# Kernel optimization log

Measured on AMD Instinct MI355X. Metric: run time of the kernel, lower is better.

## Reference

```python
import jax, jax.numpy as jnp
import numpy as np

B = 16384  # batch size
NP = 49    # 7x7 patches


def _attn(Q, K, V):
    # Faithful to the torch loop: token[i] = Q[i].T @ K[i] / sqrt(S) @ V[i].T, then permute.
    # Note dk = Q.size(1) == 49 (seq len), NOT the head dim — preserved here.
    scale = 1.0 / jnp.asarray(Q.shape[1], Q.dtype) ** 0.5  # 1/7
    S = jnp.einsum('bsd,bse->bde', Q, K) * scale           # (B, d, d)
    # (S @ V^T)^T  ->  out[b,s,d] = sum_e S[b,d,e] * V[b,s,e]
    return jnp.einsum('bde,bse->bsd', S, V)                # (B, 49, d)


def setup_inputs() -> dict:
    key = jax.random.key(0)
    ks = jax.random.split(key, 12)
    s = 0.1  # init scale for weights
    return {
        'x':       jax.random.normal(ks[0], (B, 3, 28, 28), dtype=jnp.float32),
        'pos_emb': jax.random.uniform(ks[1], (7, 7, 16), dtype=jnp.float32),  # torch.rand
        'WQ1': jax.random.normal(ks[2], (NP, 16, 32), dtype=jnp.float32) * s,
        'WK1': jax.random.normal(ks[3], (NP, 16, 32), dtype=jnp.float32) * s,
        'WV1': jax.random.normal(ks[4], (NP, 16, 32), dtype=jnp.float32) * s,
        'WQ2': jax.random.normal(ks[5], (NP, 8, 16), dtype=jnp.float32) * s,
        'WK2': jax.random.normal(ks[6], (NP, 8, 16), dtype=jnp.float32) * s,
        'WV2': jax.random.normal(ks[7], (NP, 8, 16), dtype=jnp.float32) * s,
        'fc1_w': jax.random.normal(ks[8], (16, NP * 8), dtype=jnp.float32) * s,
        'fc1_b': jnp.zeros((16,), dtype=jnp.float32),
        'fc2_w': jax.random.normal(ks[9], (10, 16), dtype=jnp.float32) * s,
        'fc2_b': jnp.zeros((10,), dtype=jnp.float32),
    }


def reference(x, pos_emb, WQ1, WK1, WV1, WQ2, WK2, WV2, fc1_w, fc1_b, fc2_w, fc2_b):
    b = x.shape[0]
    # grayscale (x has 3 channels)
    g = 0.299 * x[:, 0] + 0.587 * x[:, 1] + 0.114 * x[:, 2]   # (B, 28, 28)
    # 7x7 grid of 4x4 patches, flattened row-major within each patch
    patches = g.reshape(b, 7, 4, 7, 4).transpose(0, 1, 3, 2, 4).reshape(b, NP, 16)
    pe = jnp.broadcast_to(pos_emb.reshape(1, NP, 16), (b, NP, 16))
    tok1 = jnp.concatenate([patches, pe], axis=-1)            # (B, 49, 32)

    # 49 independent per-patch projections, batched: y[:,s,:] = tok[:,s,:] @ W[s].T
    Q1 = jnp.einsum('bsi,soi->bso', tok1, WQ1)
    K1 = jnp.einsum('bsi,soi->bso', tok1, WK1)
    V1 = jnp.einsum('bsi,soi->bso', tok1, WV1)
    tok2 = jax.nn.softmax(_attn(Q1, K1, V1), axis=-1)         # (B, 49, 16)

    Q2 = jnp.einsum('bsi,soi->bso', tok2, WQ2)
    K2 = jnp.einsum('bsi,soi->bso', tok2, WK2)
    V2 = jnp.einsum('bsi,soi->bso', tok2, WV2)
    tok3 = jax.nn.softmax(_attn(Q2, K2, V2), axis=-1)         # (B, 49, 8)

    flat = tok3.reshape(b, NP * 8)
    h = jax.nn.relu(flat @ fc1_w.T + fc1_b)
    return jax.nn.softmax(h @ fc2_w.T + fc2_b, axis=-1)       # (B, 10)
```

## Files before the change

kernel.cpp:

```cpp
#include <hip/hip_runtime.h>
#include <cstdint>

typedef unsigned int u32;
typedef unsigned short u16;
typedef _Float16 h2 __attribute__((ext_vector_type(2)));

#define WS_W1A   0
#define WS_W1B   37632
#define WS_CQ    75264
#define WS_W2A   84672
#define WS_W2B   103488
#define WS_F1H   122304
#define WS_F1B   134848
#define WS_F2W   134912
#define WS_F2B   135552

__device__ __forceinline__ u32 packh2(float a, float b) {
  h2 h; h.x = (_Float16)a; h.y = (_Float16)b;
  return __builtin_bit_cast(u32, h);
}
__device__ __forceinline__ float dot2u(u32 a, u32 b, float c) {
#if __has_builtin(__builtin_amdgcn_fdot2)
  return __builtin_amdgcn_fdot2(__builtin_bit_cast(h2, a), __builtin_bit_cast(h2, b), c, false);
#else
  h2 ha = __builtin_bit_cast(h2, a), hb = __builtin_bit_cast(h2, b);
  return c + (float)ha.x * (float)hb.x + (float)ha.y * (float)hb.y;
#endif
}
__device__ __forceinline__ float dot16(const u32* t, uint4 a, uint4 b, float c) {
  c = dot2u(t[0], a.x, c); c = dot2u(t[1], a.y, c);
  c = dot2u(t[2], a.z, c); c = dot2u(t[3], a.w, c);
  c = dot2u(t[4], b.x, c); c = dot2u(t[5], b.y, c);
  c = dot2u(t[6], b.z, c); c = dot2u(t[7], b.w, c);
  return c;
}

__device__ __forceinline__ void wfence() {
  __builtin_amdgcn_sched_barrier(0);
  asm volatile("s_waitcnt lgkmcnt(0)" ::: "memory");
  __builtin_amdgcn_sched_barrier(0);
}

extern "C" __global__ void vit_prep(
    const float* __restrict__ pe,
    const float* __restrict__ wq1, const float* __restrict__ wk1, const float* __restrict__ wv1,
    const float* __restrict__ wq2, const float* __restrict__ wk2, const float* __restrict__ wv2,
    const float* __restrict__ fw1, const float* __restrict__ fb1,
    const float* __restrict__ fw2, const float* __restrict__ fb2,
    char* __restrict__ ws)
{
  const int t = blockIdx.x * 256 + threadIdx.x;
  _Float16* w1aH = (_Float16*)(ws + WS_W1A);
  _Float16* w1bH = (_Float16*)(ws + WS_W1B);
  float*    cq   = (float*)(ws + WS_CQ);
  _Float16* w2aH = (_Float16*)(ws + WS_W2A);
  _Float16* w2bH = (_Float16*)(ws + WS_W2B);
  u32* f1h = (u32*)(ws + WS_F1H);
  float* o1b = (float*)(ws + WS_F1B);
  float* o2w = (float*)(ws + WS_F2W);
  float* o2b = (float*)(ws + WS_F2B);

  if (t < 2352) {
    int p = t / 784, rem = t % 784;
    int o = rem / 49, s = rem % 49;
    const float* W = (p == 0 ? wq1 : (p == 1 ? wk1 : wv1)) + s*512 + o*32;
    float sc = (p == 0) ? (1.0f/7.0f) : 1.0f;
    #pragma unroll
    for (int i = 0; i < 8; ++i) w1aH[t*8 + i] = (_Float16)(W[i] * sc);
    #pragma unroll
    for (int i = 0; i < 8; ++i) w1bH[t*8 + i] = (_Float16)(W[8 + i] * sc);
    float acc = 0.f;
    #pragma unroll
    for (int i = 0; i < 16; ++i) acc += pe[s*16 + i] * W[16 + i];
    cq[t] = acc * sc;
  } else if (t < 3528) {
    int u = t - 2352;
    int p = u / 392, rem = u % 392;
    int o = rem / 49, s = rem % 49;
    const float* W = (p == 0 ? wq2 : (p == 1 ? wk2 : wv2)) + s*128 + o*16;
    float sc = (p == 0) ? (1.0f/7.0f) : 1.0f;
    #pragma unroll
    for (int i = 0; i < 8; ++i) w2aH[u*8 + i] = (_Float16)(W[i] * sc);
    #pragma unroll
    for (int i = 0; i < 8; ++i) w2bH[u*8 + i] = (_Float16)(W[8 + i] * sc);
  } else if (t < 6664) {
    int u = t - 3528;
    int h = u / 196, jc = u % 196;
    f1h[u] = packh2(fw1[h*392 + 2*jc], fw1[h*392 + 2*jc + 1]);
  } else if (t < 6680) {
    int u = t - 6664; o1b[u] = fb1[u];
  } else if (t < 6840) {
    int u = t - 6680; o2w[u] = fw2[u];
  } else if (t < 6850) {
    int u = t - 6840; o2b[u] = fb2[u];
  }
}

extern "C" __global__ void __launch_bounds__(256, 2)
vit_main(const float* __restrict__ x, const char* __restrict__ ws, float* __restrict__ out)
{
  __shared__ uint4 smem4[32768 / 16];
  char* smem = (char*)smem4;
  const u32 tid  = threadIdx.x;
  const u32 lane = tid & 63u;
  const u32 wv   = tid >> 6;

  const uint4* g1a = (const uint4*)(ws + WS_W1A);
  const uint4* g1b = (const uint4*)(ws + WS_W1B);
  const float* gcq = (const float*)(ws + WS_CQ);
  const uint4* g2a = (const uint4*)(ws + WS_W2A);
  const uint4* g2b = (const uint4*)(ws + WS_W2B);
  const uint4* f1hg = (const uint4*)(ws + WS_F1H);
  const float* f1bg = (const float*)(ws + WS_F1B);
  const float* f2wg = (const float*)(ws + WS_F2W);
  const float* f2bg = (const float*)(ws + WS_F2B);

  char* pw = smem + wv * 8192;
  const u32 s = lane;
  const u32 pr = s / 7u, pc = s - pr * 7u;

  const u32 bbase = blockIdx.x * 8u + wv * 2u;

  u32 p2h[2][8];
  u32 v1h[2][8];
  u32 th4[2][8];
  u32 v2h[2][4];

  if (s < 49u) {
    #pragma unroll
    for (int u = 0; u < 2; ++u) {
      const float* xb = x + (size_t)(bbase + u) * 2352u;
      #pragma unroll
      for (int r = 0; r < 4; ++r) {
        const float* rp = xb + (4u*pr + r) * 28u + 4u*pc;
        float4 rr = *(const float4*)rp;
        float4 gg = *(const float4*)(rp + 784);
        float4 bb = *(const float4*)(rp + 1568);
        float g0 = 0.299f*rr.x + 0.587f*gg.x + 0.114f*bb.x;
        float g1 = 0.299f*rr.y + 0.587f*gg.y + 0.114f*bb.y;
        float g2 = 0.299f*rr.z + 0.587f*gg.z + 0.114f*bb.z;
        float g3 = 0.299f*rr.w + 0.587f*gg.w + 0.114f*bb.w;
        p2h[u][r*2]   = packh2(g0, g1);
        p2h[u][r*2+1] = packh2(g2, g3);
      }
    }
  }

  if (s < 49u) {
    const int si = (int)s;
    uint4 qa0, qb0, qa1, qb1; float qc0, qc1;
    uint4 ka0, kb0, ka1, kb1; float kc0, kc1;
    uint4 va0, vb0, va1, vb1; float vc0, vc1;
#define LDQ1(OP) { const int r0 = (OP)*98 + si;        qa0=g1a[r0]; qb0=g1b[r0]; qa1=g1a[r0+49]; qb1=g1b[r0+49]; qc0=gcq[r0]; qc1=gcq[r0+49]; }
#define LDK1(OP) { const int r0 = (OP)*98 + si + 784;  ka0=g1a[r0]; kb0=g1b[r0]; ka1=g1a[r0+49]; kb1=g1b[r0+49]; kc0=gcq[r0]; kc1=gcq[r0+49]; }
#define LDV1(OP) { const int r0 = (OP)*98 + si + 1568; va0=g1a[r0]; vb0=g1b[r0]; va1=g1a[r0+49]; vb1=g1b[r0+49]; vc0=gcq[r0]; vc1=gcq[r0+49]; }
    LDQ1(0); LDK1(0); LDV1(0);
    #pragma unroll
    for (int op = 0; op < 8; ++op) {
      const int o = 2*op;
      {
        #pragma unroll
        for (int u = 0; u < 2; ++u) {
          _Float16* qrow = (_Float16*)(pw + u*4096);
          qrow[o*56 + s]     = (_Float16)dot16(p2h[u], qa0, qb0, qc0);
          qrow[(o+1)*56 + s] = (_Float16)dot16(p2h[u], qa1, qb1, qc1);
        }
      }
      if (op < 7) LDQ1(op+1);
      {
        #pragma unroll
        for (int u = 0; u < 2; ++u) {
          _Float16* krow = (_Float16*)(pw + u*4096 + 1792);
          krow[o*56 + s]     = (_Float16)dot16(p2h[u], ka0, kb0, kc0);
          krow[(o+1)*56 + s] = (_Float16)dot16(p2h[u], ka1, kb1, kc1);
        }
      }
      if (op < 7) LDK1(op+1);
      {
        #pragma unroll
        for (int u = 0; u < 2; ++u)
          v1h[u][op] = packh2(dot16(p2h[u], va0, vb0, vc0), dot16(p2h[u], va1, vb1, vc1));
      }
      if (op < 7) LDV1(op+1);
    }
#undef LDQ1
#undef LDK1
#undef LDV1
  }
  wfence();

  {
    const u32 d2 = lane >> 3, e2 = lane & 7u;
    #pragma unroll
    for (int u = 0; u < 2; ++u) {
      char* su = pw + u*4096;
      const u32* qw = (const u32*)su;
      const u32* kw = (const u32*)(su + 1792);
      const u32* qA = qw + (2u*d2) * 28u;
      const u32* qB = qA + 28u;
      const u32* kA = kw + (2u*e2) * 28u;
      const u32* kB = kA + 28u;
      float a00 = 0.f, a01 = 0.f, a10 = 0.f, a11 = 0.f;
      #pragma unroll
      for (int t7 = 0; t7 < 6; ++t7) {
        uint4 qa = *(const uint4*)(qA + 4*t7);
        uint4 qb = *(const uint4*)(qB + 4*t7);
        uint4 ka = *(const uint4*)(kA + 4*t7);
        uint4 kb = *(const uint4*)(kB + 4*t7);
        a00 = dot2u(qa.x, ka.x, a00); a00 = dot2u(qa.y, ka.y, a00);
        a00 = dot2u(qa.z, ka.z, a00); a00 = dot2u(qa.w, ka.w, a00);
        a01 = dot2u(qa.x, kb.x, a01); a01 = dot2u(qa.y, kb.y, a01);
        a01 = dot2u(qa.z, kb.z, a01); a01 = dot2u(qa.w, kb.w, a01);
        a10 = dot2u(qb.x, ka.x, a10); a10 = dot2u(qb.y, ka.y, a10);
        a10 = dot2u(qb.z, ka.z, a10); a10 = dot2u(qb.w, ka.w, a10);
        a11 = dot2u(qb.x, kb.x, a11); a11 = dot2u(qb.y, kb.y, a11);
        a11 = dot2u(qb.z, kb.z, a11); a11 = dot2u(qb.w, kb.w, a11);
      }
      {
        float q0t = (float)((const _Float16*)qA)[48];
        float q1t = (float)((const _Float16*)qB)[48];
        float k0t = (float)((const _Float16*)kA)[48];
        float k1t = (float)((const _Float16*)kB)[48];
        a00 = fmaf(q0t, k0t, a00); a01 = fmaf(q0t, k1t, a01);
        a10 = fmaf(q1t, k0t, a10); a11 = fmaf(q1t, k1t, a11);
      }
      u32* s1 = (u32*)(su + 3584);
      s1[(2u*d2)*8u + e2]   = packh2(a00, a01);
      s1[(2u*d2+1)*8u + e2] = packh2(a10, a11);
    }
  }
  wfence();

  if (s < 49u) {
    #pragma unroll
    for (int u = 0; u < 2; ++u) {
      char* su = pw + u*4096;
      const u32* s1 = (const u32*)(su + 3584);
      float od[16];
      #pragma unroll
      for (int d = 0; d < 16; ++d) {
        uint4 sa = *(const uint4*)&s1[d*8];
        uint4 sb = *(const uint4*)&s1[d*8 + 4];
        float acc = dot2u(sa.x, v1h[u][0], 0.f);
        acc = dot2u(sa.y, v1h[u][1], acc);
        acc = dot2u(sa.z, v1h[u][2], acc);
        acc = dot2u(sa.w, v1h[u][3], acc);
        acc = dot2u(sb.x, v1h[u][4], acc);
        acc = dot2u(sb.y, v1h[u][5], acc);
        acc = dot2u(sb.z, v1h[u][6], acc);
        acc = dot2u(sb.w, v1h[u][7], acc);
        od[d] = acc;
      }
      float m = od[0];
      #pragma unroll
      for (int d = 1; d < 16; ++d) m = fmaxf(m, od[d]);
      float sum = 0.f;
      #pragma unroll
      for (int d = 0; d < 16; ++d) { od[d] = __expf(od[d] - m); sum += od[d]; }
      float rs = 1.0f / sum;
      #pragma unroll
      for (int j = 0; j < 8; ++j) th4[u][j] = packh2(od[2*j]*rs, od[2*j+1]*rs);
    }
  }

  if (s < 49u) {
    const int si = (int)s;
    uint4 qa0, qb0, qa1, qb1;
    uint4 ka0, kb0, ka1, kb1;
    uint4 va0, vb0, va1, vb1;
#define LDQ2(OP) { const int r0 = (OP)*98 + si;       qa0=g2a[r0]; qb0=g2b[r0]; qa1=g2a[r0+49]; qb1=g2b[r0+49]; }
#define LDK2(OP) { const int r0 = (OP)*98 + si + 392; ka0=g2a[r0]; kb0=g2b[r0]; ka1=g2a[r0+49]; kb1=g2b[r0+49]; }
#define LDV2(OP) { const int r0 = (OP)*98 + si + 784; va0=g2a[r0]; vb0=g2b[r0]; va1=g2a[r0+49]; vb1=g2b[r0+49]; }
    LDQ2(0); LDK2(0); LDV2(0);
    #pragma unroll
    for (int op = 0; op < 4; ++op) {
      const int o = 2*op;
      {
        #pragma unroll
        for (int u = 0; u < 2; ++u) {
          _Float16* qrow = (_Float16*)(pw + u*4096);
          qrow[o*56 + s]     = (_Float16)dot16(th4[u], qa0, qb0, 0.f);
          qrow[(o+1)*56 + s] = (_Float16)dot16(th4[u], qa1, qb1, 0.f);
        }
      }
      if (op < 3) LDQ2(op+1);
      {
        #pragma unroll
        for (int u = 0; u < 2; ++u) {
          _Float16* krow = (_Float16*)(pw + u*4096 + 896);
          krow[o*56 + s]     = (_Float16)dot16(th4[u], ka0, kb0, 0.f);
          krow[(o+1)*56 + s] = (_Float16)dot16(th4[u], ka1, kb1, 0.f);
        }
      }
      if (op < 3) LDK2(op+1);
      {
        #pragma unroll
        for (int u = 0; u < 2; ++u)
          v2h[u][op] = packh2(dot16(th4[u], va0, vb0, 0.f), dot16(th4[u], va1, vb1, 0.f));
      }
      if (op < 3) LDV2(op+1);
    }
#undef LDQ2
#undef LDK2
#undef LDV2
  }
  wfence();

  {
    const u32 uu = lane >> 5, d = (lane >> 2) & 7u, e2 = lane & 3u;
    char* su = pw + uu*4096;
    const u32* qw = (const u32*)su;
    const u32* kw = (const u32*)(su + 896);
    const u32* qA = qw + d * 28u;
    const u32* kA = kw + (2u*e2) * 28u;
    const u32* kB = kA + 28u;
    float a0 = 0.f, a1 = 0.f;
    #pragma unroll
    for (int t7 = 0; t7 < 6; ++t7) {
      uint4 qa = *(const uint4*)(qA + 4*t7);
      uint4 ka = *(const uint4*)(kA + 4*t7);
      uint4 kb = *(const uint4*)(kB + 4*t7);
      a0 = dot2u(qa.x, ka.x, a0); a0 = dot2u(qa.y, ka.y, a0);
      a0 = dot2u(qa.z, ka.z, a0); a0 = dot2u(qa.w, ka.w, a0);
      a1 = dot2u(qa.x, kb.x, a1); a1 = dot2u(qa.y, kb.y, a1);
      a1 = dot2u(qa.z, kb.z, a1); a1 = dot2u(qa.w, kb.w, a1);
    }
    {
      float qt = (float)((const _Float16*)qA)[48];
      float k0t = (float)((const _Float16*)kA)[48];
      float k1t = (float)((const _Float16*)kB)[48];
      a0 = fmaf(qt, k0t, a0); a1 = fmaf(qt, k1t, a1);
    }
    u32* s2 = (u32*)(su + 3584);
    s2[d*4u + e2] = packh2(a0, a1);
  }
  wfence();

  if (s < 49u) {
    #pragma unroll
    for (int u = 0; u < 2; ++u) {
      char* su = pw + u*4096;
      const u32* s2 = (const u32*)(su + 3584);
      float od[8];
      #pragma unroll
      for (int d = 0; d < 8; ++d) {
        uint4 sr = *(const uint4*)&s2[d*4];
        float acc = dot2u(sr.x, v2h[u][0], 0.f);
        acc = dot2u(sr.y, v2h[u][1], acc);
        acc = dot2u(sr.z, v2h[u][2], acc);
        acc = dot2u(sr.w, v2h[u][3], acc);
        od[d] = acc;
      }
      float m = od[0];
      #pragma unroll
      for (int d = 1; d < 8; ++d) m = fmaxf(m, od[d]);
      float sum = 0.f;
      #pragma unroll
      for (int d = 0; d < 8; ++d) { od[d] = __expf(od[d] - m); sum += od[d]; }
      float rs = 1.0f / sum;
      uint4 tw;
      tw.x = packh2(od[0]*rs, od[1]*rs);
      tw.y = packh2(od[2]*rs, od[3]*rs);
      tw.z = packh2(od[4]*rs, od[5]*rs);
      tw.w = packh2(od[6]*rs, od[7]*rs);
      *(uint4*)((u32*)su + s*4u) = tw;
    }
  }
  wfence();

  {
    const u32 uu = lane >> 5, h = (lane >> 1) & 15u, half = lane & 1u;
    char* su = pw + uu*4096;
    const u32* t3 = (const u32*)su;
    float acc = half ? 0.f : f1bg[h];
    #pragma unroll
    for (int jj = 0; jj < 25; ++jj) {
      int j = (int)(half * 25u) + jj;
      if (j < 49) {
        uint4 tj = *(const uint4*)&t3[j*4];
        uint4 wj = f1hg[h*49u + (u32)j];
        acc = dot2u(tj.x, wj.x, acc);
        acc = dot2u(tj.y, wj.y, acc);
        acc = dot2u(tj.z, wj.z, acc);
        acc = dot2u(tj.w, wj.w, acc);
      }
    }
    float* prt = (float*)(su + 3584 + 192);
    prt[h*2u + half] = acc;
  }
  wfence();

  {
    const u32 uu = lane >> 5, c = lane & 31u;
    char* su = pw + uu*4096;
    if (c < 10u) {
      const float4* pv4 = (const float4*)(su + 3584 + 192);
      float hb[16];
      #pragma unroll
      for (int g = 0; g < 8; ++g) {
        float4 pv = pv4[g];
        hb[2*g]   = fmaxf(pv.x + pv.y, 0.f);
        hb[2*g+1] = fmaxf(pv.z + pv.w, 0.f);
      }
      const float* wr = f2wg + c*16u;
      float acc = f2bg[c];
      #pragma unroll
      for (int h = 0; h < 16; ++h) acc = fmaf(hb[h], wr[h], acc);
      float* lg = (float*)(su + 3584 + 384);
      lg[c] = acc;
    }
  }
  wfence();

  {
    const u32 uu = lane >> 5, c = lane & 31u;
    char* su = pw + uu*4096;
    if (c < 10u) {
      const float* lg = (const float*)(su + 3584 + 384);
      float mx = lg[0];
      #pragma unroll
      for (int i = 1; i < 10; ++i) mx = fmaxf(mx, lg[i]);
      float sum = 0.f;
      #pragma unroll
      for (int i = 0; i < 10; ++i) sum += __expf(lg[i] - mx);
      out[(size_t)(bbase + uu) * 10u + c] = __expf(lg[c] - mx) / sum;
    }
  }
}

extern "C" void kernel_launch(void* const* d_in, const int* in_sizes, int n_in,
                              void* d_out, int out_size, void* d_ws, size_t ws_size,
                              hipStream_t stream)
{
  const float* x   = (const float*)d_in[0];
  const float* pe  = (const float*)d_in[1];
  const float* wq1 = (const float*)d_in[2];
  const float* wk1 = (const float*)d_in[3];
  const float* wv1 = (const float*)d_in[4];
  const float* wq2 = (const float*)d_in[5];
  const float* wk2 = (const float*)d_in[6];
  const float* wv2 = (const float*)d_in[7];
  const float* f1w = (const float*)d_in[8];
  const float* f1b = (const float*)d_in[9];
  const float* f2w = (const float*)d_in[10];
  const float* f2b = (const float*)d_in[11];
  char* ws = (char*)d_ws;
  float* out = (float*)d_out;

  hipLaunchKernelGGL(vit_prep, dim3(27), dim3(256), 0, stream,
                     pe, wq1, wk1, wv1, wq2, wk2, wv2, f1w, f1b, f2w, f2b, ws);
  hipLaunchKernelGGL(vit_main, dim3(2048), dim3(256), 0, stream, x, ws, out);
}
```

Measured before the change: 282.6 us.

## Process one sample per wavefront to cut registers and raise occupancy

```diff
diff --git a/kernel.cpp b/kernel.cpp
--- a/kernel.cpp
+++ b/kernel.cpp
@@ -96,10 +96,10 @@
   }
 }
 
-extern "C" __global__ void __launch_bounds__(256, 2)
+extern "C" __global__ void __launch_bounds__(256, 8)
 vit_main(const float* __restrict__ x, const char* __restrict__ ws, float* __restrict__ out)
 {
-  __shared__ uint4 smem4[32768 / 16];
+  __shared__ uint4 smem4[16384 / 16];
   char* smem = (char*)smem4;
   const u32 tid  = threadIdx.x;
   const u32 lane = tid & 63u;
@@ -115,34 +115,31 @@
   const float* f2wg = (const float*)(ws + WS_F2W);
   const float* f2bg = (const float*)(ws + WS_F2B);
 
-  char* pw = smem + wv * 8192;
+  char* su = smem + wv * 4096;
   const u32 s = lane;
   const u32 pr = s / 7u, pc = s - pr * 7u;
 
-  const u32 bbase = blockIdx.x * 8u + wv * 2u;
-
-  u32 p2h[2][8];
-  u32 v1h[2][8];
-  u32 th4[2][8];
-  u32 v2h[2][4];
-
-  if (s < 49u) {
-    #pragma unroll
-    for (int u = 0; u < 2; ++u) {
-      const float* xb = x + (size_t)(bbase + u) * 2352u;
-      #pragma unroll
-      for (int r = 0; r < 4; ++r) {
-        const float* rp = xb + (4u*pr + r) * 28u + 4u*pc;
-        float4 rr = *(const float4*)rp;
-        float4 gg = *(const float4*)(rp + 784);
-        float4 bb = *(const float4*)(rp + 1568);
-        float g0 = 0.299f*rr.x + 0.587f*gg.x + 0.114f*bb.x;
-        float g1 = 0.299f*rr.y + 0.587f*gg.y + 0.114f*bb.y;
-        float g2 = 0.299f*rr.z + 0.587f*gg.z + 0.114f*bb.z;
-        float g3 = 0.299f*rr.w + 0.587f*gg.w + 0.114f*bb.w;
-        p2h[u][r*2]   = packh2(g0, g1);
-        p2h[u][r*2+1] = packh2(g2, g3);
-      }
+  const u32 bbase = blockIdx.x * 4u + wv;
+
+  u32 p2h[8];
+  u32 v1h[8];
+  u32 th4[8];
+  u32 v2h[4];
+
+  if (s < 49u) {
+    const float* xb = x + (size_t)bbase * 2352u;
+    #pragma unroll
+    for (int r = 0; r < 4; ++r) {
+      const float* rp = xb + (4u*pr + r) * 28u + 4u*pc;
+      float4 rr = *(const float4*)rp;
+      float4 gg = *(const float4*)(rp + 784);
+      float4 bb = *(const float4*)(rp + 1568);
+      float g0 = 0.299f*rr.x + 0.587f*gg.x + 0.114f*bb.x;
+      float g1 = 0.299f*rr.y + 0.587f*gg.y + 0.114f*bb.y;
+      float g2 = 0.299f*rr.z + 0.587f*gg.z + 0.114f*bb.z;
+      float g3 = 0.299f*rr.w + 0.587f*gg.w + 0.114f*bb.w;
+      p2h[r*2]   = packh2(g0, g1);
+      p2h[r*2+1] = packh2(g2, g3);
     }
   }
 
@@ -155,32 +152,18 @@
 #define LDK1(OP) { const int r0 = (OP)*98 + si + 784;  ka0=g1a[r0]; kb0=g1b[r0]; ka1=g1a[r0+49]; kb1=g1b[r0+49]; kc0=gcq[r0]; kc1=gcq[r0+49]; }
 #define LDV1(OP) { const int r0 = (OP)*98 + si + 1568; va0=g1a[r0]; vb0=g1b[r0]; va1=g1a[r0+49]; vb1=g1b[r0+49]; vc0=gcq[r0]; vc1=gcq[r0+49]; }
     LDQ1(0); LDK1(0); LDV1(0);
+    _Float16* qrow = (_Float16*)su;
+    _Float16* krow = (_Float16*)(su + 1792);
     #pragma unroll
     for (int op = 0; op < 8; ++op) {
       const int o = 2*op;
-      {
-        #pragma unroll
-        for (int u = 0; u < 2; ++u) {
-          _Float16* qrow = (_Float16*)(pw + u*4096);
-          qrow[o*56 + s]     = (_Float16)dot16(p2h[u], qa0, qb0, qc0);
-          qrow[(o+1)*56 + s] = (_Float16)dot16(p2h[u], qa1, qb1, qc1);
-        }
-      }
+      qrow[o*56 + s]     = (_Float16)dot16(p2h, qa0, qb0, qc0);
+      qrow[(o+1)*56 + s] = (_Float16)dot16(p2h, qa1, qb1, qc1);
       if (op < 7) LDQ1(op+1);
-      {
-        #pragma unroll
-        for (int u = 0; u < 2; ++u) {
-          _Float16* krow = (_Float16*)(pw + u*4096 + 1792);
-          krow[o*56 + s]     = (_Float16)dot16(p2h[u], ka0, kb0, kc0);
-          krow[(o+1)*56 + s] = (_Float16)dot16(p2h[u], ka1, kb1, kc1);
-        }
-      }
+      krow[o*56 + s]     = (_Float16)dot16(p2h, ka0, kb0, kc0);
+      krow[(o+1)*56 + s] = (_Float16)dot16(p2h, ka1, kb1, kc1);
       if (op < 7) LDK1(op+1);
-      {
-        #pragma unroll
-        for (int u = 0; u < 2; ++u)
-          v1h[u][op] = packh2(dot16(p2h[u], va0, vb0, vc0), dot16(p2h[u], va1, vb1, vc1));
-      }
+      v1h[op] = packh2(dot16(p2h, va0, vb0, vc0), dot16(p2h, va1, vb1, vc1));
       if (op < 7) LDV1(op+1);
     }
 #undef LDQ1
@@ -191,76 +174,68 @@
 
   {
     const u32 d2 = lane >> 3, e2 = lane & 7u;
-    #pragma unroll
-    for (int u = 0; u < 2; ++u) {
-      char* su = pw + u*4096;
-      const u32* qw = (const u32*)su;
-      const u32* kw = (const u32*)(su + 1792);
-      const u32* qA = qw + (2u*d2) * 28u;
-      const u32* qB = qA + 28u;
-      const u32* kA = kw + (2u*e2) * 28u;
-      const u32* kB = kA + 28u;
-      float a00 = 0.f, a01 = 0.f, a10 = 0.f, a11 = 0.f;
-      #pragma unroll
-      for (int t7 = 0; t7 < 6; ++t7) {
-        uint4 qa = *(const uint4*)(qA + 4*t7);
-        uint4 qb = *(const uint4*)(qB + 4*t7);
-        uint4 ka = *(const uint4*)(kA + 4*t7);
-        uint4 kb = *(const uint4*)(kB + 4*t7);
-        a00 = dot2u(qa.x, ka.x, a00); a00 = dot2u(qa.y, ka.y, a00);
-        a00 = dot2u(qa.z, ka.z, a00); a00 = dot2u(qa.w, ka.w, a00);
-        a01 = dot2u(qa.x, kb.x, a01); a01 = dot2u(qa.y, kb.y, a01);
-        a01 = dot2u(qa.z, kb.z, a01); a01 = dot2u(qa.w, kb.w, a01);
-        a10 = dot2u(qb.x, ka.x, a10); a10 = dot2u(qb.y, ka.y, a10);
-        a10 = dot2u(qb.z, ka.z, a10); a10 = dot2u(qb.w, ka.w, a10);
-        a11 = dot2u(qb.x, kb.x, a11); a11 = dot2u(qb.y, kb.y, a11);
-        a11 = dot2u(qb.z, kb.z, a11); a11 = dot2u(qb.w, kb.w, a11);
-      }
-      {
-        float q0t = (float)((const _Float16*)qA)[48];
-        float q1t = (float)((const _Float16*)qB)[48];
-        float k0t = (float)((const _Float16*)kA)[48];
-        float k1t = (float)((const _Float16*)kB)[48];
-        a00 = fmaf(q0t, k0t, a00); a01 = fmaf(q0t, k1t, a01);
-        a10 = fmaf(q1t, k0t, a10); a11 = fmaf(q1t, k1t, a11);
-      }
-      u32* s1 = (u32*)(su + 3584);
-      s1[(2u*d2)*8u + e2]   = packh2(a00, a01);
-      s1[(2u*d2+1)*8u + e2] = packh2(a10, a11);
-    }
-  }
-  wfence();
-
-  if (s < 49u) {
-    #pragma unroll
-    for (int u = 0; u < 2; ++u) {
-      char* su = pw + u*4096;
-      const u32* s1 = (const u32*)(su + 3584);
-      float od[16];
-      #pragma unroll
-      for (int d = 0; d < 16; ++d) {
-        uint4 sa = *(const uint4*)&s1[d*8];
-        uint4 sb = *(const uint4*)&s1[d*8 + 4];
-        float acc = dot2u(sa.x, v1h[u][0], 0.f);
-        acc = dot2u(sa.y, v1h[u][1], acc);
-        acc = dot2u(sa.z, v1h[u][2], acc);
-        acc = dot2u(sa.w, v1h[u][3], acc);
-        acc = dot2u(sb.x, v1h[u][4], acc);
-        acc = dot2u(sb.y, v1h[u][5], acc);
-        acc = dot2u(sb.z, v1h[u][6], acc);
-        acc = dot2u(sb.w, v1h[u][7], acc);
-        od[d] = acc;
-      }
-      float m = od[0];
-      #pragma unroll
-      for (int d = 1; d < 16; ++d) m = fmaxf(m, od[d]);
-      float sum = 0.f;
-      #pragma unroll
-      for (int d = 0; d < 16; ++d) { od[d] = __expf(od[d] - m); sum += od[d]; }
-      float rs = 1.0f / sum;
-      #pragma unroll
-      for (int j = 0; j < 8; ++j) th4[u][j] = packh2(od[2*j]*rs, od[2*j+1]*rs);
-    }
+    const u32* qw = (const u32*)su;
+    const u32* kw = (const u32*)(su + 1792);
+    const u32* qA = qw + (2u*d2) * 28u;
+    const u32* qB = qA + 28u;
+    const u32* kA = kw + (2u*e2) * 28u;
+    const u32* kB = kA + 28u;
+    float a00 = 0.f, a01 = 0.f, a10 = 0.f, a11 = 0.f;
+    #pragma unroll
+    for (int t7 = 0; t7 < 6; ++t7) {
+      uint4 qa = *(const uint4*)(qA + 4*t7);
+      uint4 qb = *(const uint4*)(qB + 4*t7);
+      uint4 ka = *(const uint4*)(kA + 4*t7);
+      uint4 kb = *(const uint4*)(kB + 4*t7);
+      a00 = dot2u(qa.x, ka.x, a00); a00 = dot2u(qa.y, ka.y, a00);
+      a00 = dot2u(qa.z, ka.z, a00); a00 = dot2u(qa.w, ka.w, a00);
+      a01 = dot2u(qa.x, kb.x, a01); a01 = dot2u(qa.y, kb.y, a01);
+      a01 = dot2u(qa.z, kb.z, a01); a01 = dot2u(qa.w, kb.w, a01);
+      a10 = dot2u(qb.x, ka.x, a10); a10 = dot2u(qb.y, ka.y, a10);
+      a10 = dot2u(qb.z, ka.z, a10); a10 = dot2u(qb.w, ka.w, a10);
+      a11 = dot2u(qb.x, kb.x, a11); a11 = dot2u(qb.y, kb.y, a11);
+      a11 = dot2u(qb.z, kb.z, a11); a11 = dot2u(qb.w, kb.w, a11);
+    }
+    {
+      float q0t = (float)((const _Float16*)qA)[48];
+      float q1t = (float)((const _Float16*)qB)[48];
+      float k0t = (float)((const _Float16*)kA)[48];
+      float k1t = (float)((const _Float16*)kB)[48];
+      a00 = fmaf(q0t, k0t, a00); a01 = fmaf(q0t, k1t, a01);
+      a10 = fmaf(q1t, k0t, a10); a11 = fmaf(q1t, k1t, a11);
+    }
+    u32* s1 = (u32*)(su + 3584);
+    s1[(2u*d2)*8u + e2]   = packh2(a00, a01);
+    s1[(2u*d2+1)*8u + e2] = packh2(a10, a11);
+  }
+  wfence();
+
+  if (s < 49u) {
+    const u32* s1 = (const u32*)(su + 3584);
+    float od[16];
+    #pragma unroll
+    for (int d = 0; d < 16; ++d) {
+      uint4 sa = *(const uint4*)&s1[d*8];
+      uint4 sb = *(const uint4*)&s1[d*8 + 4];
+      float acc = dot2u(sa.x, v1h[0], 0.f);
+      acc = dot2u(sa.y, v1h[1], acc);
+      acc = dot2u(sa.z, v1h[2], acc);
+      acc = dot2u(sa.w, v1h[3], acc);
+      acc = dot2u(sb.x, v1h[4], acc);
+      acc = dot2u(sb.y, v1h[5], acc);
+      acc = dot2u(sb.z, v1h[6], acc);
+      acc = dot2u(sb.w, v1h[7], acc);
+      od[d] = acc;
+    }
+    float m = od[0];
+    #pragma unroll
+    for (int d = 1; d < 16; ++d) m = fmaxf(m, od[d]);
+    float sum = 0.f;
+    #pragma unroll
+    for (int d = 0; d < 16; ++d) { od[d] = __expf(od[d] - m); sum += od[d]; }
+    float rs = 1.0f / sum;
+    #pragma unroll
+    for (int j = 0; j < 8; ++j) th4[j] = packh2(od[2*j]*rs, od[2*j+1]*rs);
   }
 
   if (s < 49u) {
@@ -272,32 +247,18 @@
 #define LDK2(OP) { const int r0 = (OP)*98 + si + 392; ka0=g2a[r0]; kb0=g2b[r0]; ka1=g2a[r0+49]; kb1=g2b[r0+49]; }
 #define LDV2(OP) { const int r0 = (OP)*98 + si + 784; va0=g2a[r0]; vb0=g2b[r0]; va1=g2a[r0+49]; vb1=g2b[r0+49]; }
     LDQ2(0); LDK2(0); LDV2(0);
+    _Float16* qrow = (_Float16*)su;
+    _Float16* krow = (_Float16*)(su + 896);
     #pragma unroll
     for (int op = 0; op < 4; ++op) {
       const int o = 2*op;
-      {
-        #pragma unroll
-        for (int u = 0; u < 2; ++u) {
-          _Float16* qrow = (_Float16*)(pw + u*4096);
-          qrow[o*56 + s]     = (_Float16)dot16(th4[u], qa0, qb0, 0.f);
-          qrow[(o+1)*56 + s] = (_Float16)dot16(th4[u], qa1, qb1, 0.f);
-        }
-      }
+      qrow[o*56 + s]     = (_Float16)dot16(th4, qa0, qb0, 0.f);
+      qrow[(o+1)*56 + s] = (_Float16)dot16(th4, qa1, qb1, 0.f);
       if (op < 3) LDQ2(op+1);
-      {
-        #pragma unroll
-        for (int u = 0; u < 2; ++u) {
-          _Float16* krow = (_Float16*)(pw + u*4096 + 896);
-          krow[o*56 + s]     = (_Float16)dot16(th4[u], ka0, kb0, 0.f);
-          krow[(o+1)*56 + s] = (_Float16)dot16(th4[u], ka1, kb1, 0.f);
-        }
-      }
+      krow[o*56 + s]     = (_Float16)dot16(th4, ka0, kb0, 0.f);
+      krow[(o+1)*56 + s] = (_Float16)dot16(th4, ka1, kb1, 0.f);
       if (op < 3) LDK2(op+1);
-      {
-        #pragma unroll
-        for (int u = 0; u < 2; ++u)
-          v2h[u][op] = packh2(dot16(th4[u], va0, vb0, 0.f), dot16(th4[u], va1, vb1, 0.f));
-      }
+      v2h[op] = packh2(dot16(th4, va0, vb0, 0.f), dot16(th4, va1, vb1, 0.f));
       if (op < 3) LDV2(op+1);
     }
 #undef LDQ2
@@ -307,75 +268,61 @@
   wfence();
 
   {
-    const u32 uu = lane >> 5, d = (lane >> 2) & 7u, e2 = lane & 3u;
-    char* su = pw + uu*4096;
-    const u32* qw = (const u32*)su;
-    const u32* kw = (const u32*)(su + 896);
-    const u32* qA = qw + d * 28u;
-    const u32* kA = kw + (2u*e2) * 28u;
-    const u32* kB = kA + 28u;
-    float a0 = 0.f, a1 = 0.f;
+    const u32 d = lane >> 3, e = lane & 7u;
+    const u32* qA = (const u32*)su + d * 28u;
+    const u32* kA = (const u32*)(su + 896) + e * 28u;
+    float a0 = 0.f;
     #pragma unroll
     for (int t7 = 0; t7 < 6; ++t7) {
       uint4 qa = *(const uint4*)(qA + 4*t7);
       uint4 ka = *(const uint4*)(kA + 4*t7);
-      uint4 kb = *(const uint4*)(kB + 4*t7);
       a0 = dot2u(qa.x, ka.x, a0); a0 = dot2u(qa.y, ka.y, a0);
       a0 = dot2u(qa.z, ka.z, a0); a0 = dot2u(qa.w, ka.w, a0);
-      a1 = dot2u(qa.x, kb.x, a1); a1 = dot2u(qa.y, kb.y, a1);
-      a1 = dot2u(qa.z, kb.z, a1); a1 = dot2u(qa.w, kb.w, a1);
     }
     {
       float qt = (float)((const _Float16*)qA)[48];
-      float k0t = (float)((const _Float16*)kA)[48];
-      float k1t = (float)((const _Float16*)kB)[48];
-      a0 = fmaf(qt, k0t, a0); a1 = fmaf(qt, k1t, a1);
-    }
-    u32* s2 = (u32*)(su + 3584);
-    s2[d*4u + e2] = packh2(a0, a1);
-  }
-  wfence();
-
-  if (s < 49u) {
-    #pragma unroll
-    for (int u = 0; u < 2; ++u) {
-      char* su = pw + u*4096;
-      const u32* s2 = (const u32*)(su + 3584);
-      float od[8];
-      #pragma unroll
-      for (int d = 0; d < 8; ++d) {
-        uint4 sr = *(const uint4*)&s2[d*4];
-        float acc = dot2u(sr.x, v2h[u][0], 0.f);
-        acc = dot2u(sr.y, v2h[u][1], acc);
-        acc = dot2u(sr.z, v2h[u][2], acc);
-        acc = dot2u(sr.w, v2h[u][3], acc);
-        od[d] = acc;
-      }
-      float m = od[0];
-      #pragma unroll
-      for (int d = 1; d < 8; ++d) m = fmaxf(m, od[d]);
-      float sum = 0.f;
-      #pragma unroll
-      for (int d = 0; d < 8; ++d) { od[d] = __expf(od[d] - m); sum += od[d]; }
-      float rs = 1.0f / sum;
-      uint4 tw;
-      tw.x = packh2(od[0]*rs, od[1]*rs);
-      tw.y = packh2(od[2]*rs, od[3]*rs);
-      tw.z = packh2(od[4]*rs, od[5]*rs);
-      tw.w = packh2(od[6]*rs, od[7]*rs);
-      *(uint4*)((u32*)su + s*4u) = tw;
-    }
+      float kt = (float)((const _Float16*)kA)[48];
+      a0 = fmaf(qt, kt, a0);
+    }
+    ((_Float16*)(su + 3584))[d*8u + e] = (_Float16)a0;
+  }
+  wfence();
+
+  if (s < 49u) {
+    const u32* s2 = (const u32*)(su + 3584);
+    float od[8];
+    #pragma unroll
+    for (int d = 0; d < 8; ++d) {
+      uint4 sr = *(const uint4*)&s2[d*4];
+      float acc = dot2u(sr.x, v2h[0], 0.f);
+      acc = dot2u(sr.y, v2h[1], acc);
+      acc = dot2u(sr.z, v2h[2], acc);
+      acc = dot2u(sr.w, v2h[3], acc);
+      od[d] = acc;
+    }
+    float m = od[0];
+    #pragma unroll
+    for (int d = 1; d < 8; ++d) m = fmaxf(m, od[d]);
+    float sum = 0.f;
+    #pragma unroll
+    for (int d = 0; d < 8; ++d) { od[d] = __expf(od[d] - m); sum += od[d]; }
+    float rs = 1.0f / sum;
+    uint4 tw;
+    tw.x = packh2(od[0]*rs, od[1]*rs);
+    tw.y = packh2(od[2]*rs, od[3]*rs);
+    tw.z = packh2(od[4]*rs, od[5]*rs);
+    tw.w = packh2(od[6]*rs, od[7]*rs);
+    *(uint4*)((u32*)su + s*4u) = tw;
   }
   wfence();
 
   {
-    const u32 uu = lane >> 5, h = (lane >> 1) & 15u, half = lane & 1u;
-    char* su = pw + uu*4096;
+    const u32 h = lane >> 2, q = lane & 3u;
     const u32* t3 = (const u32*)su;
-    float acc = half ? 0.f : f1bg[h];
-    #pragma unroll
-    for (int jj = 0; jj < 25; ++jj) {
-      int j = (int)(half * 25u) + jj;
+    float acc = (q == 0u) ? f1bg[h] : 0.f;
+    #pragma unroll
+    for (int jj = 0; jj < 13; ++jj) {
+      int j = (int)(q * 13u) + jj;
       if (j < 49) {
         uint4 tj = *(const uint4*)&t3[j*4];
         uint4 wj = f1hg[h*49u + (u32)j];
@@ -385,46 +332,34 @@
         acc = dot2u(tj.w, wj.w, acc);
       }
     }
-    float* prt = (float*)(su + 3584 + 192);
-    prt[h*2u + half] = acc;
+    acc += __shfl_xor(acc, 1, 64);
+    acc += __shfl_xor(acc, 2, 64);
+    float hv = fmaxf(acc, 0.f);
+    if (q == 0u) ((float*)(su + 3584))[h] = hv;
   }
   wfence();
 
   {
-    const u32 uu = lane >> 5, c = lane & 31u;
-    char* su = pw + uu*4096;
-    if (c < 10u) {
-      const float4* pv4 = (const float4*)(su + 3584 + 192);
-      float hb[16];
-      #pragma unroll
-      for (int g = 0; g < 8; ++g) {
-        float4 pv = pv4[g];
-        hb[2*g]   = fmaxf(pv.x + pv.y, 0.f);
-        hb[2*g+1] = fmaxf(pv.z + pv.w, 0.f);
-      }
-      const float* wr = f2wg + c*16u;
-      float acc = f2bg[c];
-      #pragma unroll
-      for (int h = 0; h < 16; ++h) acc = fmaf(hb[h], wr[h], acc);
-      float* lg = (float*)(su + 3584 + 384);
-      lg[c] = acc;
-    }
-  }
-  wfence();
-
-  {
-    const u32 uu = lane >> 5, c = lane & 31u;
-    char* su = pw + uu*4096;
-    if (c < 10u) {
-      const float* lg = (const float*)(su + 3584 + 384);
-      float mx = lg[0];
-      #pragma unroll
-      for (int i = 1; i < 10; ++i) mx = fmaxf(mx, lg[i]);
-      float sum = 0.f;
-      #pragma unroll
-      for (int i = 0; i < 10; ++i) sum += __expf(lg[i] - mx);
-      out[(size_t)(bbase + uu) * 10u + c] = __expf(lg[c] - mx) / sum;
-    }
+    const u32 c = lane & 15u;
+    const float* hbp = (const float*)(su + 3584);
+    const u32 cs = (c < 10u) ? c : 0u;
+    const float* wr = f2wg + cs*16u;
+    float acc = f2bg[cs];
+    #pragma unroll
+    for (int h = 0; h < 16; ++h) acc = fmaf(hbp[h], wr[h], acc);
+    float v = (c < 10u) ? acc : -__builtin_inff();
+    float mx = v;
+    mx = fmaxf(mx, __shfl_xor(mx, 1, 16));
+    mx = fmaxf(mx, __shfl_xor(mx, 2, 16));
+    mx = fmaxf(mx, __shfl_xor(mx, 4, 16));
+    mx = fmaxf(mx, __shfl_xor(mx, 8, 16));
+    float e = __expf(v - mx);
+    float sm = e;
+    sm += __shfl_xor(sm, 1, 16);
+    sm += __shfl_xor(sm, 2, 16);
+    sm += __shfl_xor(sm, 4, 16);
+    sm += __shfl_xor(sm, 8, 16);
+    if (lane < 10u) out[(size_t)bbase * 10u + lane] = e / sm;
   }
 }
 
@@ -449,5 +384,5 @@
 
   hipLaunchKernelGGL(vit_prep, dim3(27), dim3(256), 0, stream,
                      pe, wq1, wk1, wv1, wq2, wk2, wv2, f1w, f1b, f2w, f2b, ws);
-  hipLaunchKernelGGL(vit_main, dim3(2048), dim3(256), 0, stream, x, ws, out);
-}
+  hipLaunchKernelGGL(vit_main, dim3(4096), dim3(256), 0, stream, x, ws, out);
+}
```

Result: slower. 364.8 us (+29.1%).
